# Kernel tuning notes

Measured on AMD Instinct MI355X. Metric: run time of the kernel, lower is better.

Reference implementation:

```python
import jax, jax.numpy as jnp
import numpy as np

B, S, HID = 2, 2048, 2048
NH, NKV, D = 16, 4, 128  # heads, kv heads, dim_per_head
ROPE_BASE = 10000.0


def setup_inputs() -> dict:
    key = jax.random.key(0)
    ks = jax.random.split(key, 5)
    x = jax.random.normal(ks[0], (B, S, HID), jnp.float32)
    wq = jax.random.normal(ks[1], (HID, NH * D), jnp.float32) * 0.02
    wk = jax.random.normal(ks[2], (HID, NKV * D), jnp.float32) * 0.02
    wv = jax.random.normal(ks[3], (HID, NKV * D), jnp.float32) * 0.02
    wo = jax.random.normal(ks[4], (NH * D, HID), jnp.float32) * 0.02
    inv_freq = 1.0 / (ROPE_BASE ** (jnp.arange(0, D, 2, dtype=jnp.float32) / D))
    freqs = jnp.outer(jnp.arange(S, dtype=jnp.float32), inv_freq)  # [S, D/2]
    cos, sin = jnp.cos(freqs), jnp.sin(freqs)
    mask = jnp.tril(jnp.ones((S, S), dtype=bool))  # causal, True = attend
    return {"x": x, "wq": wq, "wk": wk, "wv": wv, "wo": wo,
            "cos": cos, "sin": sin, "mask": mask}


def _rope_interleave(t, cos, sin):
    # t: [B, H, S, D]; cos/sin: [S, D/2]; interleaved pairs (even, odd)
    te, to = t[..., ::2], t[..., 1::2]
    c, s = cos[None, None], sin[None, None]
    re = te * c - to * s
    ro = to * c + te * s
    return jnp.stack([re, ro], axis=-1).reshape(t.shape)


def reference(x, wq, wk, wv, wo, cos, sin, mask):
    b, s, _ = x.shape
    # QKV projections + shape(): [B, S, hid] -> [B, H, S, D]
    q = (x @ wq).reshape(b, s, NH, D).transpose(0, 2, 1, 3)
    k = (x @ wk).reshape(b, s, NKV, D).transpose(0, 2, 1, 3)
    v = (x @ wv).reshape(b, s, NKV, D).transpose(0, 2, 1, 3)
    q = _rope_interleave(q, cos, sin)
    k = _rope_interleave(k, cos, sin)
    # GQA: repeat each kv head heads//heads_kv times consecutively
    rep = NH // NKV
    k = jnp.repeat(k, rep, axis=1)
    v = jnp.repeat(v, rep, axis=1)
    scores = jnp.einsum('bhqd,bhkd->bhqk', q, k) * (D ** -0.5)
    scores = scores.astype(jnp.float32)
    scores = jnp.where(mask[None, None], scores, jnp.finfo(jnp.float32).min)
    attn = jax.nn.softmax(scores, axis=-1).astype(x.dtype)
    ctx = jnp.einsum('bhqk,bhkd->bhqd', attn, v)
    ctx = ctx.transpose(0, 2, 1, 3).reshape(b, s, NH * D)  # unshape()
    return ctx @ wo
```

## Files before the change

kernel.cpp:

```cpp
#include <hip/hip_runtime.h>
#include <hip/hip_bf16.h>
#include <math.h>

#define S_LEN 2048
#define HIDW 2048
#define NHEAD 16
#define NKVH 4
#define HD 128
#define NB 2
#define MROWS (NB * S_LEN)
#define QKVN (NHEAD * HD + 2 * NKVH * HD)
#define KOFF (NHEAD * HD)
#define VOFF (NHEAD * HD + NKVH * HD)

typedef __bf16 bf16_t;
typedef __bf16 bf16x8_t __attribute__((ext_vector_type(8)));
typedef float f32x4_t __attribute__((ext_vector_type(4)));

__device__ __forceinline__ void gload_lds16(const bf16_t* g, bf16_t* l) {
  __builtin_amdgcn_global_load_lds(
      (const __attribute__((address_space(1))) void*)g,
      (__attribute__((address_space(3))) void*)l, 16, 0, 0);
}

__device__ __forceinline__ f32x4_t zero4() {
  f32x4_t z = {0.f, 0.f, 0.f, 0.f};
  return z;
}

__device__ __forceinline__ float fexp2(float x) {
#if __has_builtin(__builtin_amdgcn_exp2f)
  return __builtin_amdgcn_exp2f(x);
#else
  return exp2f(x);
#endif
}

__global__ __launch_bounds__(256) void k_cvt8(const float* __restrict__ in,
                                              bf16_t* __restrict__ out, int n8) {
  int i = blockIdx.x * 256 + threadIdx.x;
  if (i >= n8) return;
  const float4* p = (const float4*)(in + (size_t)i * 8);
  float4 a = p[0], b = p[1];
  bf16x8_t r;
  r[0] = (bf16_t)a.x; r[1] = (bf16_t)a.y; r[2] = (bf16_t)a.z; r[3] = (bf16_t)a.w;
  r[4] = (bf16_t)b.x; r[5] = (bf16_t)b.y; r[6] = (bf16_t)b.z; r[7] = (bf16_t)b.w;
  *(bf16x8_t*)(out + (size_t)i * 8) = r;
}

__global__ __launch_bounds__(256) void k_tr_cvt(const float* __restrict__ in,
                                                bf16_t* __restrict__ out, int R, int C) {
  __shared__ float t[32][33];
  int c0 = blockIdx.x * 32, r0 = blockIdx.y * 32;
  int tx = threadIdx.x & 31, ty = threadIdx.x >> 5;
#pragma unroll
  for (int rr = ty; rr < 32; rr += 8) t[rr][tx] = in[(size_t)(r0 + rr) * C + c0 + tx];
  __syncthreads();
#pragma unroll
  for (int rr = ty; rr < 32; rr += 8)
    out[(size_t)(c0 + rr) * R + r0 + tx] = (bf16_t)t[tx][rr];
}

__global__ __launch_bounds__(512, 2) void k_gemm_qkv(const bf16_t* __restrict__ A,
                                                     const bf16_t* __restrict__ Bt,
                                                     bf16_t* __restrict__ qkv,
                                                     const float* __restrict__ cosT,
                                                     const float* __restrict__ sinT) {
  __shared__ bf16_t As[2][256 * 64];
  __shared__ bf16_t Bs[2][192 * 64];
  const int K = HIDW;
  int tid = threadIdx.x;
  int lane = tid & 63, wid = tid >> 6;
  int l15 = lane & 15, lg = lane >> 4;
  int wrb = (wid >> 2) * 128;
  int wcb = (wid & 3) * 48;

  int nwg = gridDim.x;
  int qx = nwg >> 3;
  int lin = blockIdx.x;
  int wg = (lin & 7) * qx + (lin >> 3);
  int row0 = (wg >> 4) * 256, col0 = (wg & 15) * 192;

  int srow = tid >> 3;
  int scol = ((tid & 7) ^ (srow & 7)) * 8;
  const bf16_t* Ag = A + (size_t)(row0 + srow) * K + scol;
  const bf16_t* Bg = Bt + (size_t)(col0 + srow) * K + scol;

  f32x4_t acc[8][3];
#pragma unroll
  for (int i = 0; i < 8; i++)
#pragma unroll
    for (int j = 0; j < 3; j++) acc[i][j] = zero4();

  int xr = (l15 & 7) << 4;
  const int nk = K >> 6;

  auto stA = [&](int tt, int u) {
    gload_lds16(Ag + (size_t)u * 64 * K + (size_t)tt * 64, As[tt & 1] + u * 4096 + tid * 8);
  };
  auto stB = [&](int tt, int u) {
    gload_lds16(Bg + (size_t)u * 64 * K + (size_t)tt * 64, Bs[tt & 1] + u * 4096 + tid * 8);
  };

  for (int tt = 0; tt < 2; tt++) {
    for (int u = 0; u < 4; u++) stA(tt, u);
    for (int u = 0; u < 3; u++) stB(tt, u);
  }
  asm volatile("s_waitcnt vmcnt(7)" ::: "memory");
  __builtin_amdgcn_s_barrier();
  __builtin_amdgcn_sched_barrier(0);

  for (int t = 0; t < nk; t++) {
    const char* Ac = (const char*)As[t & 1];
    const char* Bc = (const char*)Bs[t & 1];
    bool pf = (t + 2 < nk);

    bf16x8_t af0[4][2], bfr[3][2];
#pragma unroll
    for (int i = 0; i < 4; i++) {
      int row = wrb + i * 16 + l15;
#pragma unroll
      for (int kk = 0; kk < 2; kk++)
        af0[i][kk] = *(const bf16x8_t*)(Ac + ((row * 128 + kk * 64 + lg * 16) ^ xr));
    }
#pragma unroll
    for (int j = 0; j < 3; j++) {
      int rowb = wcb + j * 16 + l15;
#pragma unroll
      for (int kk = 0; kk < 2; kk++)
        bfr[j][kk] = *(const bf16x8_t*)(Bc + ((rowb * 128 + kk * 64 + lg * 16) ^ xr));
    }
    __builtin_amdgcn_s_barrier();
    __builtin_amdgcn_s_setprio(1);
#pragma unroll
    for (int i = 0; i < 4; i++)
#pragma unroll
      for (int j = 0; j < 2; j++)
#pragma unroll
        for (int kk = 0; kk < 2; kk++)
          acc[i][j] = __builtin_amdgcn_mfma_f32_16x16x32_bf16(af0[i][kk], bfr[j][kk],
                                                              acc[i][j], 0, 0, 0);
    __builtin_amdgcn_s_setprio(0);

    if (pf) { stA(t + 2, 0); stA(t + 2, 2); }
    __builtin_amdgcn_s_barrier();
    __builtin_amdgcn_s_setprio(1);
#pragma unroll
    for (int i = 0; i < 4; i++)
#pragma unroll
      for (int kk = 0; kk < 2; kk++)
        acc[i][2] = __builtin_amdgcn_mfma_f32_16x16x32_bf16(af0[i][kk], bfr[2][kk],
                                                            acc[i][2], 0, 0, 0);
    __builtin_amdgcn_s_setprio(0);

    bf16x8_t af1[4][2];
#pragma unroll
    for (int i = 0; i < 4; i++) {
      int row = wrb + 64 + i * 16 + l15;
#pragma unroll
      for (int kk = 0; kk < 2; kk++)
        af1[i][kk] = *(const bf16x8_t*)(Ac + ((row * 128 + kk * 64 + lg * 16) ^ xr));
    }
    if (pf) { stB(t + 2, 0); stB(t + 2, 1); }
    __builtin_amdgcn_s_barrier();
    __builtin_amdgcn_s_setprio(1);
#pragma unroll
    for (int i = 0; i < 4; i++)
#pragma unroll
      for (int j = 0; j < 2; j++)
#pragma unroll
        for (int kk = 0; kk < 2; kk++)
          acc[4 + i][j] = __builtin_amdgcn_mfma_f32_16x16x32_bf16(
              af1[i][kk], bfr[j][kk], acc[4 + i][j], 0, 0, 0);
    __builtin_amdgcn_s_setprio(0);

    if (pf) { stB(t + 2, 2); stA(t + 2, 1); stA(t + 2, 3); }
    __builtin_amdgcn_s_barrier();
    __builtin_amdgcn_s_setprio(1);
#pragma unroll
    for (int i = 0; i < 4; i++)
#pragma unroll
      for (int kk = 0; kk < 2; kk++)
        acc[4 + i][2] = __builtin_amdgcn_mfma_f32_16x16x32_bf16(
            af1[i][kk], bfr[2][kk], acc[4 + i][2], 0, 0, 0);
    __builtin_amdgcn_s_setprio(0);

    if (t + 1 < nk) {
      if (pf) asm volatile("s_waitcnt vmcnt(7)" ::: "memory");
      else    asm volatile("s_waitcnt vmcnt(0)" ::: "memory");
    }
    __builtin_amdgcn_s_barrier();
    __builtin_amdgcn_sched_barrier(0);
  }

  if (col0 < VOFF) {
    int sbase = row0 & (S_LEN - 1);
    const float QS = 0.08838834764831845f * 1.4426950408889634f;
#pragma unroll
    for (int hh = 0; hh < 2; hh++) {
      const float* cp = cosT + (size_t)(sbase + hh * 128) * 64;
      const float* sp = sinT + (size_t)(sbase + hh * 128) * 64;
#pragma unroll
      for (int k = 0; k < 4; k++) {
        gload_lds16((const bf16_t*)(cp + k * 2048 + (size_t)tid * 4),
                    As[0] + k * 4096 + tid * 8);
        gload_lds16((const bf16_t*)(sp + k * 2048 + (size_t)tid * 4),
                    As[1] + k * 4096 + tid * 8);
      }
      asm volatile("s_waitcnt vmcnt(0)" ::: "memory");
      __builtin_amdgcn_s_barrier();
      if ((wrb >> 7) == hh) {
        const float* cosF = (const float*)As[0];
        const float* sinF = (const float*)As[1];
#pragma unroll
        for (int i = 0; i < 8; i++) {
#pragma unroll
          for (int j = 0; j < 3; j++) {
            int c = col0 + wcb + j * 16 + l15;
            int rll = i * 16 + lg * 4;
            if (c < VOFF) {
              float scale = (c < KOFF) ? QS : 1.0f;
              int p0 = (c & 127) >> 1;
              int codd = c & 1;
#pragma unroll
              for (int qd = 0; qd < 4; qd++) {
                float self = acc[i][j][qd];
                float other = __shfl_xor(self, 1);
                float cv = cosF[(rll + qd) * 64 + p0], sv = sinF[(rll + qd) * 64 + p0];
                float outv = codd ? (self * cv + other * sv) : (self * cv - other * sv);
                qkv[(size_t)(row0 + hh * 128 + rll + qd) * QKVN + c] =
                    (bf16_t)(outv * scale);
              }
            } else {
#pragma unroll
              for (int qd = 0; qd < 4; qd++)
                qkv[(size_t)(row0 + hh * 128 + rll + qd) * QKVN + c] =
                    (bf16_t)acc[i][j][qd];
            }
          }
        }
      }
      __builtin_amdgcn_s_barrier();
    }
  } else {
#pragma unroll
    for (int i = 0; i < 8; i++) {
#pragma unroll
      for (int j = 0; j < 3; j++) {
        int r = row0 + wrb + i * 16 + lg * 4;
        int c = col0 + wcb + j * 16 + l15;
#pragma unroll
        for (int qd = 0; qd < 4; qd++)
          qkv[(size_t)(r + qd) * QKVN + c] = (bf16_t)acc[i][j][qd];
      }
    }
  }
}

__global__ __launch_bounds__(512, 2) void k_gemm_out(const bf16_t* __restrict__ A,
                                                     const bf16_t* __restrict__ Bt,
                                                     float* __restrict__ Cout) {
  __shared__ bf16_t As[2][128 * 64];
  __shared__ bf16_t Bs[2][256 * 64];
  const int K = KOFF;
  const int N = HIDW;
  int tid = threadIdx.x;
  int lane = tid & 63, wid = tid >> 6;
  int l15 = lane & 15, lg = lane >> 4;
  int wrb = (wid >> 2) * 64;
  int wcb = (wid & 3) * 64;

  int nwg = gridDim.x;
  int qx = nwg >> 3;
  int lin = blockIdx.x;
  int wg = (lin & 7) * qx + (lin >> 3);
  int row0 = (wg >> 3) * 128, col0 = (wg & 7) * 256;

  int srow = tid >> 3;
  int scol = ((tid & 7) ^ (srow & 7)) * 8;
  const bf16_t* Ag = A + (size_t)(row0 + srow) * K + scol;
  const bf16_t* Bg = Bt + (size_t)(col0 + srow) * K + scol;

  f32x4_t acc[4][4];
#pragma unroll
  for (int i = 0; i < 4; i++)
#pragma unroll
    for (int j = 0; j < 4; j++) acc[i][j] = zero4();

  int xr = (l15 & 7) << 4;
  const int nk = K >> 6;

  auto stA = [&](int tt, int u) {
    gload_lds16(Ag + (size_t)u * 64 * K + (size_t)tt * 64, As[tt & 1] + u * 4096 + tid * 8);
  };
  auto stB = [&](int tt, int u) {
    gload_lds16(Bg + (size_t)u * 64 * K + (size_t)tt * 64, Bs[tt & 1] + u * 4096 + tid * 8);
  };

  for (int tt = 0; tt < 2; tt++) {
    for (int u = 0; u < 2; u++) stA(tt, u);
    for (int u = 0; u < 4; u++) stB(tt, u);
  }
  asm volatile("s_waitcnt vmcnt(6)" ::: "memory");
  __builtin_amdgcn_s_barrier();
  __builtin_amdgcn_sched_barrier(0);

  for (int t = 0; t < nk; t++) {
    const char* Ac = (const char*)As[t & 1];
    const char* Bc = (const char*)Bs[t & 1];
    bool pf = (t + 2 < nk);

    bf16x8_t af0[4][2], bfr[4][2];
#pragma unroll
    for (int i = 0; i < 4; i++) {
      int row = wrb + i * 16 + l15;
#pragma unroll
      for (int kk = 0; kk < 2; kk++)
        af0[i][kk] = *(const bf16x8_t*)(Ac + ((row * 128 + kk * 64 + lg * 16) ^ xr));
    }
#pragma unroll
    for (int j = 0; j < 4; j++) {
      int rowb = wcb + j * 16 + l15;
#pragma unroll
      for (int kk = 0; kk < 2; kk++)
        bfr[j][kk] = *(const bf16x8_t*)(Bc + ((rowb * 128 + kk * 64 + lg * 16) ^ xr));
    }
    __builtin_amdgcn_s_barrier();
    __builtin_amdgcn_s_setprio(1);
#pragma unroll
    for (int i = 0; i < 4; i++)
#pragma unroll
      for (int kk = 0; kk < 2; kk++)
        acc[i][0] = __builtin_amdgcn_mfma_f32_16x16x32_bf16(af0[i][kk], bfr[0][kk],
                                                            acc[i][0], 0, 0, 0);
    __builtin_amdgcn_s_setprio(0);

    if (pf) { stA(t + 2, 0); stA(t + 2, 1); }
    __builtin_amdgcn_s_barrier();
    __builtin_amdgcn_s_setprio(1);
#pragma unroll
    for (int i = 0; i < 4; i++)
#pragma unroll
      for (int kk = 0; kk < 2; kk++)
        acc[i][1] = __builtin_amdgcn_mfma_f32_16x16x32_bf16(af0[i][kk], bfr[1][kk],
                                                            acc[i][1], 0, 0, 0);
    __builtin_amdgcn_s_setprio(0);

    if (pf) { stB(t + 2, 0); stB(t + 2, 1); }
    __builtin_amdgcn_s_barrier();
    __builtin_amdgcn_s_setprio(1);
#pragma unroll
    for (int i = 0; i < 4; i++)
#pragma unroll
      for (int kk = 0; kk < 2; kk++)
        acc[i][2] = __builtin_amdgcn_mfma_f32_16x16x32_bf16(af0[i][kk], bfr[2][kk],
                                                            acc[i][2], 0, 0, 0);
    __builtin_amdgcn_s_setprio(0);

    if (pf) { stB(t + 2, 2); stB(t + 2, 3); }
    __builtin_amdgcn_s_barrier();
    __builtin_amdgcn_s_setprio(1);
#pragma unroll
    for (int i = 0; i < 4; i++)
#pragma unroll
      for (int kk = 0; kk < 2; kk++)
        acc[i][3] = __builtin_amdgcn_mfma_f32_16x16x32_bf16(af0[i][kk], bfr[3][kk],
                                                            acc[i][3], 0, 0, 0);
    __builtin_amdgcn_s_setprio(0);

    if (t + 1 < nk) {
      if (pf) asm volatile("s_waitcnt vmcnt(6)" ::: "memory");
      else    asm volatile("s_waitcnt vmcnt(0)" ::: "memory");
    }
    __builtin_amdgcn_s_barrier();
    __builtin_amdgcn_sched_barrier(0);
  }

#pragma unroll
  for (int i = 0; i < 4; i++) {
#pragma unroll
    for (int j = 0; j < 4; j++) {
      int r = row0 + wrb + i * 16 + lg * 4;
      int c = col0 + wcb + j * 16 + l15;
#pragma unroll
      for (int qd = 0; qd < 4; qd++)
        Cout[(size_t)(r + qd) * N + c] = acc[i][j][qd];
    }
  }
}

__global__ __launch_bounds__(256) void k_vt(const bf16_t* __restrict__ qkv,
                                            bf16_t* __restrict__ vt) {
  __shared__ bf16_t t[32][33];
  int s0 = blockIdx.x * 32;
  int dt = (blockIdx.y & 3) * 32;
  int h = blockIdx.y >> 2;
  int b = blockIdx.z;
  int tx = threadIdx.x & 31, ty = threadIdx.x >> 5;
#pragma unroll
  for (int rr = ty; rr < 32; rr += 8)
    t[rr][tx] = qkv[(size_t)(b * S_LEN + s0 + rr) * QKVN + VOFF + h * HD + dt + tx];
  __syncthreads();
#pragma unroll
  for (int rr = ty; rr < 32; rr += 8)
    vt[((size_t)((b * NKVH + h) * HD + dt + rr)) * S_LEN + s0 + tx] = t[tx][rr];
}

__global__ __launch_bounds__(256, 2) void k_attn(const bf16_t* __restrict__ qkv,
                                                 const bf16_t* __restrict__ vt,
                                                 bf16_t* __restrict__ ctx) {
  __shared__ bf16_t Ks[2 * 64 * 128];
  __shared__ bf16_t Vs[2 * 128 * 64];
  __shared__ bf16_t plds[4][16 * 72];

  int tid = threadIdx.x;
  int lane = tid & 63, wid = tid >> 6;
  int idx = blockIdx.x;
  int bh = idx & 31;
  int qg = 31 - (idx >> 5);
  int b = bh >> 4, h = bh & 15;
  int kvh = h >> 2;
  int q0 = qg * 64 + wid * 16;
  int l15 = lane & 15, lg = lane >> 4;

  const bf16_t* Kbase = qkv + (size_t)(b * S_LEN) * QKVN + KOFF + kvh * HD;
  const bf16_t* Vbase = vt + (size_t)(b * NKVH + kvh) * HD * S_LEN;

  const bf16_t* Qp = qkv + (size_t)(b * S_LEN + q0 + l15) * QKVN + h * HD + lg * 8;
  bf16x8_t aq[4];
#pragma unroll
  for (int kk = 0; kk < 4; kk++) aq[kk] = *(const bf16x8_t*)(Qp + kk * 32);

  int Ls[4], Lk[4], Lv[4];
#pragma unroll
  for (int u = 0; u < 4; u++) {
    int L = u * 4096 + tid * 16;
    Ls[u] = L >> 1;
    Lk[u] = L ^ (((L >> 8) & 7) << 4);
    Lv[u] = L ^ (((L >> 7) & 7) << 4);
  }

  f32x4_t o[8];
#pragma unroll
  for (int j = 0; j < 8; j++) o[j] = zero4();
  float ms = -INFINITY, lsum = 0.f;

  bf16_t* pbuf = &plds[wid][0];
  int xr = (l15 & 7) << 4;
  int ntiles = qg + 1;
  int qcol = q0 + l15;

#pragma unroll
  for (int u = 0; u < 4; u++) {
    gload_lds16(Kbase + (size_t)(Lk[u] >> 8) * QKVN + ((Lk[u] & 255) >> 1), Ks + Ls[u]);
    gload_lds16(Vbase + (size_t)(Lv[u] >> 7) * S_LEN + ((Lv[u] & 127) >> 1), Vs + Ls[u]);
  }
  __syncthreads();

  for (int t = 0; t < ntiles; t++) {
    int kv0 = t * 64;
    if (t + 1 < ntiles) {
      const bf16_t* Kn = Kbase + (size_t)(kv0 + 64) * QKVN;
      const bf16_t* Vn = Vbase + kv0 + 64;
      int bo = ((t + 1) & 1) * 8192;
#pragma unroll
      for (int u = 0; u < 4; u++) {
        gload_lds16(Kn + (size_t)(Lk[u] >> 8) * QKVN + ((Lk[u] & 255) >> 1), Ks + bo + Ls[u]);
        gload_lds16(Vn + (size_t)(Lv[u] >> 7) * S_LEN + ((Lv[u] & 127) >> 1), Vs + bo + Ls[u]);
      }
    }
    const char* Kb = (const char*)Ks + (t & 1) * 16384;
    const char* Vb = (const char*)Vs + (t & 1) * 16384;

    f32x4_t sacc[4];
#pragma unroll
    for (int cg = 0; cg < 4; cg++) sacc[cg] = zero4();
#pragma unroll
    for (int cg = 0; cg < 4; cg++) {
#pragma unroll
      for (int kk = 0; kk < 4; kk++) {
        int boff = ((cg * 16 + l15) * 256 + kk * 64 + lg * 16) ^ xr;
        bf16x8_t bk = *(const bf16x8_t*)(Kb + boff);
        sacc[cg] = __builtin_amdgcn_mfma_f32_16x16x32_bf16(bk, aq[kk], sacc[cg], 0, 0, 0);
      }
    }
    if (kv0 + 63 > q0) {
#pragma unroll
      for (int cg = 0; cg < 4; cg++) {
#pragma unroll
        for (int i = 0; i < 4; i++) {
          int kvg = kv0 + cg * 16 + lg * 4 + i;
          if (kvg > qcol) sacc[cg][i] = -1e30f;
        }
      }
    }
    float pmax = sacc[0][0];
#pragma unroll
    for (int cg = 0; cg < 4; cg++)
#pragma unroll
      for (int i = 0; i < 4; i++) pmax = fmaxf(pmax, sacc[cg][i]);
    pmax = fmaxf(pmax, __shfl_xor(pmax, 16));
    pmax = fmaxf(pmax, __shfl_xor(pmax, 32));
    if (__any(pmax - ms > 8.0f)) {
      float nm = fmaxf(ms, pmax);
      float sc = fexp2(ms - nm);
      ms = nm;
      lsum *= sc;
      float sci[4];
#pragma unroll
      for (int i = 0; i < 4; i++) sci[i] = __shfl(sc, lg * 4 + i);
#pragma unroll
      for (int j = 0; j < 8; j++)
#pragma unroll
        for (int i = 0; i < 4; i++) o[j][i] *= sci[i];
    }
    float ls = 0.f;
#pragma unroll
    for (int cg = 0; cg < 4; cg++)
#pragma unroll
      for (int i = 0; i < 4; i++) {
        sacc[cg][i] = fexp2(sacc[cg][i] - ms);
        ls += sacc[cg][i];
      }
    ls += __shfl_xor(ls, 16);
    ls += __shfl_xor(ls, 32);
    lsum += ls;
#pragma unroll
    for (int cg = 0; cg < 4; cg++)
#pragma unroll
      for (int i = 0; i < 4; i++)
        pbuf[l15 * 72 + cg * 16 + lg * 4 + i] = (bf16_t)sacc[cg][i];
    __builtin_amdgcn_wave_barrier();
    bf16x8_t pa0 = *(const bf16x8_t*)(pbuf + l15 * 72 + lg * 8);
    bf16x8_t pa1 = *(const bf16x8_t*)(pbuf + l15 * 72 + 32 + lg * 8);
    __builtin_amdgcn_wave_barrier();
#pragma unroll
    for (int j = 0; j < 8; j++) {
      int d = j * 16 + l15;
      int bo0 = (d * 128 + lg * 16) ^ xr;
      int bo1 = (d * 128 + 64 + lg * 16) ^ xr;
      o[j] = __builtin_amdgcn_mfma_f32_16x16x32_bf16(
          pa0, *(const bf16x8_t*)(Vb + bo0), o[j], 0, 0, 0);
      o[j] = __builtin_amdgcn_mfma_f32_16x16x32_bf16(
          pa1, *(const bf16x8_t*)(Vb + bo1), o[j], 0, 0, 0);
    }
    __syncthreads();
  }

  bf16_t* Cp = ctx + (size_t)(b * S_LEN + q0) * KOFF + h * HD;
#pragma unroll
  for (int i = 0; i < 4; i++) {
    float inv = 1.f / __shfl(lsum, lg * 4 + i);
    int row = lg * 4 + i;
#pragma unroll
    for (int j = 0; j < 8; j++)
      Cp[(size_t)row * KOFF + j * 16 + l15] = (bf16_t)(o[j][i] * inv);
  }
}

extern "C" void kernel_launch(void* const* d_in, const int* in_sizes, int n_in,
                              void* d_out, int out_size, void* d_ws, size_t ws_size,
                              hipStream_t stream) {
  const float* x = (const float*)d_in[0];
  const float* wq = (const float*)d_in[1];
  const float* wk = (const float*)d_in[2];
  const float* wv = (const float*)d_in[3];
  const float* wo = (const float*)d_in[4];
  const float* cosT = (const float*)d_in[5];
  const float* sinT = (const float*)d_in[6];

  bf16_t* xb = (bf16_t*)d_ws;
  bf16_t* wqkvT = xb + (size_t)MROWS * HIDW;
  bf16_t* woT = wqkvT + (size_t)QKVN * HIDW;
  bf16_t* qkv = woT + (size_t)HIDW * HIDW;
  bf16_t* vtb = qkv + (size_t)MROWS * QKVN;

  k_cvt8<<<MROWS * HIDW / 8 / 256, 256, 0, stream>>>(x, xb, MROWS * HIDW / 8);
  k_tr_cvt<<<dim3(KOFF / 32, HIDW / 32), 256, 0, stream>>>(wq, wqkvT, HIDW, KOFF);
  k_tr_cvt<<<dim3((NKVH * HD) / 32, HIDW / 32), 256, 0, stream>>>(
      wk, wqkvT + (size_t)KOFF * HIDW, HIDW, NKVH * HD);
  k_tr_cvt<<<dim3((NKVH * HD) / 32, HIDW / 32), 256, 0, stream>>>(
      wv, wqkvT + (size_t)VOFF * HIDW, HIDW, NKVH * HD);
  k_tr_cvt<<<dim3(HIDW / 32, KOFF / 32), 256, 0, stream>>>(wo, woT, KOFF, HIDW);
  k_gemm_qkv<<<(MROWS / 256) * (QKVN / 192), 512, 0, stream>>>(
      xb, wqkvT, qkv, cosT, sinT);
  k_vt<<<dim3(S_LEN / 32, 4 * NKVH, NB), 256, 0, stream>>>(qkv, vtb);
  k_attn<<<32 * 32, 256, 0, stream>>>(qkv, vtb, xb);
  k_gemm_out<<<(MROWS / 128) * (HIDW / 256), 512, 0, stream>>>(xb, woT,
                                                               (float*)d_out);
}
```

Before: 201.4 us.

## Retile QKV GEMM to 256x256 tiles with split-half prefetch schedule

Replaces the 256x192 QKV projection GEMM with a 256x256 tile. The LDS buffers are split into halves that are prefetched at different stages of the K loop, with explicit lgkmcnt waits between the MFMA phases. The RoPE epilogue now loads the cos/sin tables for all 256 rows at once instead of two 128-row passes. The larger tile raises operand reuse per block, but the grid shrinks from 256 to 192 workgroups, so on a 256-CU part some CUs sit idle.

New measurement: 205.6 us. +2.1%, slower.

```diff
diff --git a/kernel.cpp b/kernel.cpp
--- a/kernel.cpp
+++ b/kernel.cpp
@@ -61,76 +61,82 @@
     out[(size_t)(c0 + rr) * R + r0 + tx] = (bf16_t)t[tx][rr];
 }
 
-__global__ __launch_bounds__(512, 2) void k_gemm_qkv(const bf16_t* __restrict__ A,
-                                                     const bf16_t* __restrict__ Bt,
-                                                     bf16_t* __restrict__ qkv,
-                                                     const float* __restrict__ cosT,
-                                                     const float* __restrict__ sinT) {
-  __shared__ bf16_t As[2][256 * 64];
-  __shared__ bf16_t Bs[2][192 * 64];
-  const int K = HIDW;
+__global__ __launch_bounds__(512, 2) void k_gemm_qkv8(const bf16_t* __restrict__ A,
+                                                      const bf16_t* __restrict__ Bt,
+                                                      bf16_t* __restrict__ qkv,
+                                                      const float* __restrict__ cosT,
+                                                      const float* __restrict__ sinT) {
+  __shared__ bf16_t As[2][16384];
+  __shared__ bf16_t Bs[2][16384];
+  const int K = HIDW, N = QKVN;
   int tid = threadIdx.x;
   int lane = tid & 63, wid = tid >> 6;
   int l15 = lane & 15, lg = lane >> 4;
   int wrb = (wid >> 2) * 128;
-  int wcb = (wid & 3) * 48;
-
-  int nwg = gridDim.x;
-  int qx = nwg >> 3;
+  int wcb = (wid & 3) * 64;
+  int ah = wid >> 2;
+  int bh2 = wcb >> 7;
+  int brow0 = wcb & 64;
+
+  int qx = gridDim.x >> 3;
   int lin = blockIdx.x;
   int wg = (lin & 7) * qx + (lin >> 3);
-  int row0 = (wg >> 4) * 256, col0 = (wg & 15) * 192;
+  int row0 = (wg / 12) * 256, col0 = (wg % 12) * 256;
 
   int srow = tid >> 3;
   int scol = ((tid & 7) ^ (srow & 7)) * 8;
   const bf16_t* Ag = A + (size_t)(row0 + srow) * K + scol;
   const bf16_t* Bg = Bt + (size_t)(col0 + srow) * K + scol;
 
-  f32x4_t acc[8][3];
+  f32x4_t acc[8][4];
 #pragma unroll
   for (int i = 0; i < 8; i++)
 #pragma unroll
-    for (int j = 0; j < 3; j++) acc[i][j] = zero4();
+    for (int j = 0; j < 4; j++) acc[i][j] = zero4();
 
   int xr = (l15 & 7) << 4;
   const int nk = K >> 6;
 
-  auto stA = [&](int tt, int u) {
-    gload_lds16(Ag + (size_t)u * 64 * K + (size_t)tt * 64, As[tt & 1] + u * 4096 + tid * 8);
+  auto stA = [&](int tt, int h, int u) {
+    gload_lds16(Ag + (size_t)(h * 128 + u * 64) * K + (size_t)tt * 64,
+                As[tt & 1] + h * 8192 + u * 4096 + tid * 8);
   };
-  auto stB = [&](int tt, int u) {
-    gload_lds16(Bg + (size_t)u * 64 * K + (size_t)tt * 64, Bs[tt & 1] + u * 4096 + tid * 8);
+  auto stB = [&](int tt, int h, int u) {
+    gload_lds16(Bg + (size_t)(h * 128 + u * 64) * K + (size_t)tt * 64,
+                Bs[tt & 1] + h * 8192 + u * 4096 + tid * 8);
   };
 
-  for (int tt = 0; tt < 2; tt++) {
-    for (int u = 0; u < 4; u++) stA(tt, u);
-    for (int u = 0; u < 3; u++) stB(tt, u);
-  }
-  asm volatile("s_waitcnt vmcnt(7)" ::: "memory");
+  stB(0, 0, 0); stB(0, 0, 1); stA(0, 0, 0); stA(0, 0, 1);
+  stB(0, 1, 0); stB(0, 1, 1); stA(0, 1, 0); stA(0, 1, 1);
+  stB(1, 0, 0); stB(1, 0, 1); stA(1, 0, 0); stA(1, 0, 1);
+  stB(1, 1, 0); stB(1, 1, 1);
+  asm volatile("s_waitcnt vmcnt(10)" ::: "memory");
   __builtin_amdgcn_s_barrier();
   __builtin_amdgcn_sched_barrier(0);
 
   for (int t = 0; t < nk; t++) {
-    const char* Ac = (const char*)As[t & 1];
-    const char* Bc = (const char*)Bs[t & 1];
-    bool pf = (t + 2 < nk);
-
-    bf16x8_t af0[4][2], bfr[3][2];
+    const char* Ac = (const char*)As[t & 1] + ah * 16384;
+    const char* Bc = (const char*)Bs[t & 1] + bh2 * 16384;
+
+    bf16x8_t af0[4][2], bfr[4][2];
 #pragma unroll
     for (int i = 0; i < 4; i++) {
-      int row = wrb + i * 16 + l15;
+      int row = i * 16 + l15;
 #pragma unroll
       for (int kk = 0; kk < 2; kk++)
         af0[i][kk] = *(const bf16x8_t*)(Ac + ((row * 128 + kk * 64 + lg * 16) ^ xr));
     }
 #pragma unroll
-    for (int j = 0; j < 3; j++) {
-      int rowb = wcb + j * 16 + l15;
-#pragma unroll
-      for (int kk = 0; kk < 2; kk++)
-        bfr[j][kk] = *(const bf16x8_t*)(Bc + ((rowb * 128 + kk * 64 + lg * 16) ^ xr));
-    }
-    __builtin_amdgcn_s_barrier();
+    for (int j = 0; j < 2; j++) {
+      int row = brow0 + j * 16 + l15;
+#pragma unroll
+      for (int kk = 0; kk < 2; kk++)
+        bfr[j][kk] = *(const bf16x8_t*)(Bc + ((row * 128 + kk * 64 + lg * 16) ^ xr));
+    }
+    if (t + 1 < nk) { stA(t + 1, 1, 0); stA(t + 1, 1, 1); }
+    __builtin_amdgcn_s_barrier();
+    asm volatile("s_waitcnt lgkmcnt(0)" ::: "memory");
+    __builtin_amdgcn_sched_barrier(0);
     __builtin_amdgcn_s_setprio(1);
 #pragma unroll
     for (int i = 0; i < 4; i++)
@@ -141,28 +147,42 @@
           acc[i][j] = __builtin_amdgcn_mfma_f32_16x16x32_bf16(af0[i][kk], bfr[j][kk],
                                                               acc[i][j], 0, 0, 0);
     __builtin_amdgcn_s_setprio(0);
-
-    if (pf) { stA(t + 2, 0); stA(t + 2, 2); }
-    __builtin_amdgcn_s_barrier();
-    __builtin_amdgcn_s_setprio(1);
-#pragma unroll
-    for (int i = 0; i < 4; i++)
-#pragma unroll
-      for (int kk = 0; kk < 2; kk++)
-        acc[i][2] = __builtin_amdgcn_mfma_f32_16x16x32_bf16(af0[i][kk], bfr[2][kk],
-                                                            acc[i][2], 0, 0, 0);
-    __builtin_amdgcn_s_setprio(0);
+    __builtin_amdgcn_s_barrier();
+
+#pragma unroll
+    for (int j = 2; j < 4; j++) {
+      int row = brow0 + j * 16 + l15;
+#pragma unroll
+      for (int kk = 0; kk < 2; kk++)
+        bfr[j][kk] = *(const bf16x8_t*)(Bc + ((row * 128 + kk * 64 + lg * 16) ^ xr));
+    }
+    __builtin_amdgcn_s_barrier();
+    asm volatile("s_waitcnt lgkmcnt(0)" ::: "memory");
+    __builtin_amdgcn_sched_barrier(0);
+    __builtin_amdgcn_s_setprio(1);
+#pragma unroll
+    for (int i = 0; i < 4; i++)
+#pragma unroll
+      for (int j = 2; j < 4; j++)
+#pragma unroll
+        for (int kk = 0; kk < 2; kk++)
+          acc[i][j] = __builtin_amdgcn_mfma_f32_16x16x32_bf16(af0[i][kk], bfr[j][kk],
+                                                              acc[i][j], 0, 0, 0);
+    __builtin_amdgcn_s_setprio(0);
+    __builtin_amdgcn_s_barrier();
 
     bf16x8_t af1[4][2];
 #pragma unroll
     for (int i = 0; i < 4; i++) {
-      int row = wrb + 64 + i * 16 + l15;
+      int row = 64 + i * 16 + l15;
 #pragma unroll
       for (int kk = 0; kk < 2; kk++)
         af1[i][kk] = *(const bf16x8_t*)(Ac + ((row * 128 + kk * 64 + lg * 16) ^ xr));
     }
-    if (pf) { stB(t + 2, 0); stB(t + 2, 1); }
-    __builtin_amdgcn_s_barrier();
+    if (t + 2 < nk) { stB(t + 2, 0, 0); stB(t + 2, 0, 1); }
+    __builtin_amdgcn_s_barrier();
+    asm volatile("s_waitcnt lgkmcnt(0)" ::: "memory");
+    __builtin_amdgcn_sched_barrier(0);
     __builtin_amdgcn_s_setprio(1);
 #pragma unroll
     for (int i = 0; i < 4; i++)
@@ -173,85 +193,72 @@
           acc[4 + i][j] = __builtin_amdgcn_mfma_f32_16x16x32_bf16(
               af1[i][kk], bfr[j][kk], acc[4 + i][j], 0, 0, 0);
     __builtin_amdgcn_s_setprio(0);
-
-    if (pf) { stB(t + 2, 2); stA(t + 2, 1); stA(t + 2, 3); }
-    __builtin_amdgcn_s_barrier();
-    __builtin_amdgcn_s_setprio(1);
-#pragma unroll
-    for (int i = 0; i < 4; i++)
-#pragma unroll
-      for (int kk = 0; kk < 2; kk++)
-        acc[4 + i][2] = __builtin_amdgcn_mfma_f32_16x16x32_bf16(
-            af1[i][kk], bfr[2][kk], acc[4 + i][2], 0, 0, 0);
-    __builtin_amdgcn_s_setprio(0);
-
-    if (t + 1 < nk) {
-      if (pf) asm volatile("s_waitcnt vmcnt(7)" ::: "memory");
-      else    asm volatile("s_waitcnt vmcnt(0)" ::: "memory");
-    }
+    __builtin_amdgcn_s_barrier();
+
+    if (t + 2 < nk) { stA(t + 2, 0, 0); stA(t + 2, 0, 1); stB(t + 2, 1, 0); stB(t + 2, 1, 1); }
+    __builtin_amdgcn_s_barrier();
+    __builtin_amdgcn_s_setprio(1);
+#pragma unroll
+    for (int i = 0; i < 4; i++)
+#pragma unroll
+      for (int j = 2; j < 4; j++)
+#pragma unroll
+        for (int kk = 0; kk < 2; kk++)
+          acc[4 + i][j] = __builtin_amdgcn_mfma_f32_16x16x32_bf16(
+              af1[i][kk], bfr[j][kk], acc[4 + i][j], 0, 0, 0);
+    __builtin_amdgcn_s_setprio(0);
+    if (t + 2 < nk) asm volatile("s_waitcnt vmcnt(10)" ::: "memory");
+    else            asm volatile("s_waitcnt vmcnt(0)" ::: "memory");
     __builtin_amdgcn_s_barrier();
     __builtin_amdgcn_sched_barrier(0);
   }
 
   if (col0 < VOFF) {
     int sbase = row0 & (S_LEN - 1);
+    bf16_t* cosL = &As[0][0];
+    bf16_t* sinL = &Bs[0][0];
+#pragma unroll
+    for (int k = 0; k < 8; k++) {
+      gload_lds16((const bf16_t*)(cosT + (size_t)sbase * 64 + k * 2048 + tid * 4),
+                  cosL + k * 4096 + tid * 8);
+      gload_lds16((const bf16_t*)(sinT + (size_t)sbase * 64 + k * 2048 + tid * 4),
+                  sinL + k * 4096 + tid * 8);
+    }
+    asm volatile("s_waitcnt vmcnt(0)" ::: "memory");
+    __builtin_amdgcn_s_barrier();
+    const float* cosF = (const float*)cosL;
+    const float* sinF = (const float*)sinL;
     const float QS = 0.08838834764831845f * 1.4426950408889634f;
 #pragma unroll
-    for (int hh = 0; hh < 2; hh++) {
-      const float* cp = cosT + (size_t)(sbase + hh * 128) * 64;
-      const float* sp = sinT + (size_t)(sbase + hh * 128) * 64;
-#pragma unroll
-      for (int k = 0; k < 4; k++) {
-        gload_lds16((const bf16_t*)(cp + k * 2048 + (size_t)tid * 4),
-                    As[0] + k * 4096 + tid * 8);
-        gload_lds16((const bf16_t*)(sp + k * 2048 + (size_t)tid * 4),
-                    As[1] + k * 4096 + tid * 8);
-      }
-      asm volatile("s_waitcnt vmcnt(0)" ::: "memory");
-      __builtin_amdgcn_s_barrier();
-      if ((wrb >> 7) == hh) {
-        const float* cosF = (const float*)As[0];
-        const float* sinF = (const float*)As[1];
-#pragma unroll
-        for (int i = 0; i < 8; i++) {
-#pragma unroll
-          for (int j = 0; j < 3; j++) {
-            int c = col0 + wcb + j * 16 + l15;
-            int rll = i * 16 + lg * 4;
-            if (c < VOFF) {
-              float scale = (c < KOFF) ? QS : 1.0f;
-              int p0 = (c & 127) >> 1;
-              int codd = c & 1;
-#pragma unroll
-              for (int qd = 0; qd < 4; qd++) {
-                float self = acc[i][j][qd];
-                float other = __shfl_xor(self, 1);
-                float cv = cosF[(rll + qd) * 64 + p0], sv = sinF[(rll + qd) * 64 + p0];
-                float outv = codd ? (self * cv + other * sv) : (self * cv - other * sv);
-                qkv[(size_t)(row0 + hh * 128 + rll + qd) * QKVN + c] =
-                    (bf16_t)(outv * scale);
-              }
-            } else {
-#pragma unroll
-              for (int qd = 0; qd < 4; qd++)
-                qkv[(size_t)(row0 + hh * 128 + rll + qd) * QKVN + c] =
-                    (bf16_t)acc[i][j][qd];
-            }
-          }
+    for (int i = 0; i < 8; i++) {
+#pragma unroll
+      for (int j = 0; j < 4; j++) {
+        int c = col0 + wcb + j * 16 + l15;
+        int rlb = wrb + ((i < 4) ? i * 16 : 64 + (i - 4) * 16) + lg * 4;
+        float scale = (c < KOFF) ? QS : 1.0f;
+        int p0 = (c & 127) >> 1;
+        int codd = c & 1;
+#pragma unroll
+        for (int qd = 0; qd < 4; qd++) {
+          int rl = rlb + qd;
+          float self = acc[i][j][qd];
+          float other = __shfl_xor(self, 1);
+          float cv = cosF[rl * 64 + p0], sv = sinF[rl * 64 + p0];
+          float outv = codd ? (self * cv + other * sv) : (self * cv - other * sv);
+          ((bf16_t*)qkv)[(size_t)(row0 + rl) * N + c] = (bf16_t)(outv * scale);
         }
       }
-      __builtin_amdgcn_s_barrier();
     }
   } else {
 #pragma unroll
     for (int i = 0; i < 8; i++) {
 #pragma unroll
-      for (int j = 0; j < 3; j++) {
-        int r = row0 + wrb + i * 16 + lg * 4;
+      for (int j = 0; j < 4; j++) {
+        int r = row0 + wrb + ((i < 4) ? i * 16 : 64 + (i - 4) * 16) + lg * 4;
         int c = col0 + wcb + j * 16 + l15;
 #pragma unroll
         for (int qd = 0; qd < 4; qd++)
-          qkv[(size_t)(r + qd) * QKVN + c] = (bf16_t)acc[i][j][qd];
+          qkv[(size_t)(r + qd) * N + c] = (bf16_t)acc[i][j][qd];
       }
     }
   }
@@ -262,16 +269,14 @@
                                                      float* __restrict__ Cout) {
   __shared__ bf16_t As[2][128 * 64];
   __shared__ bf16_t Bs[2][256 * 64];
-  const int K = KOFF;
-  const int N = HIDW;
+  const int K = KOFF, N = HIDW;
   int tid = threadIdx.x;
   int lane = tid & 63, wid = tid >> 6;
   int l15 = lane & 15, lg = lane >> 4;
   int wrb = (wid >> 2) * 64;
   int wcb = (wid & 3) * 64;
 
-  int nwg = gridDim.x;
-  int qx = nwg >> 3;
+  int qx = gridDim.x >> 3;
   int lin = blockIdx.x;
   int wg = (lin & 7) * qx + (lin >> 3);
   int row0 = (wg >> 3) * 128, col0 = (wg & 7) * 256;
@@ -582,7 +587,7 @@
   k_tr_cvt<<<dim3((NKVH * HD) / 32, HIDW / 32), 256, 0, stream>>>(
       wv, wqkvT + (size_t)VOFF * HIDW, HIDW, NKVH * HD);
   k_tr_cvt<<<dim3(HIDW / 32, KOFF / 32), 256, 0, stream>>>(wo, woT, KOFF, HIDW);
-  k_gemm_qkv<<<(MROWS / 256) * (QKVN / 192), 512, 0, stream>>>(
+  k_gemm_qkv8<<<(MROWS / 256) * (QKVN / 256), 512, 0, stream>>>(
       xb, wqkvT, qkv, cosT, sinT);
   k_vt<<<dim3(S_LEN / 32, 4 * NKVH, NB), 256, 0, stream>>>(qkv, vtb);
   k_attn<<<32 * 32, 256, 0, stream>>>(qkv, vtb, xb);
```
